# Performance work log

Measured on AMD Instinct MI355X. Metric: run time of the kernel, lower is better.

Reference implementation:

```python
import jax, jax.numpy as jnp
import numpy as np

B, S, D_IN, D_OUT = 4, 2048, 1024, 1024


def setup_inputs() -> dict:
    key = jax.random.key(0)
    ks = jax.random.split(key, 7)
    s_in = 1.0 / np.sqrt(D_IN)
    return {
        "x": jax.random.normal(ks[0], (B, S, D_IN), dtype=jnp.float32),
        "Wq": jax.random.uniform(ks[1], (D_IN, D_OUT), jnp.float32, -s_in, s_in),
        "bq": jax.random.uniform(ks[2], (D_OUT,), jnp.float32, -s_in, s_in),
        "Wk": jax.random.uniform(ks[3], (D_IN, D_OUT), jnp.float32, -s_in, s_in),
        "bk": jax.random.uniform(ks[4], (D_OUT,), jnp.float32, -s_in, s_in),
        "Wv": jax.random.uniform(ks[5], (D_IN, D_OUT), jnp.float32, -s_in, s_in),
        "bv": jax.random.uniform(ks[6], (D_OUT,), jnp.float32, -s_in, s_in),
    }


def reference(x, Wq, bq, Wk, bk, Wv, bv):
    # Linear projections (torch Linear: x @ W^T + b; here W stored as [in,out])
    q = x @ Wq + bq  # [B,S,D]
    k = x @ Wk + bk
    v = x @ Wv + bv
    scores = jnp.einsum("bqd,bkd->bqk", q, k)  # [B,S,S]
    # causal mask: positions j > i masked with -inf (applied BEFORE scaling,
    # which is equivalent since -inf/sqrt(d) == -inf)
    seq = scores.shape[-1]
    causal = jnp.tril(jnp.ones((seq, seq), dtype=bool))
    masked = jnp.where(causal, scores, -jnp.inf)
    attn = jax.nn.softmax(masked / np.sqrt(k.shape[-1]), axis=-1)
    # dropout p=0.0 -> identity
    return attn @ v  # [B,S,D]
```

## Files before the change

### kernel.cpp

```cpp
#include <hip/hip_runtime.h>

typedef unsigned short u16;
typedef unsigned int u32;
typedef __attribute__((ext_vector_type(8))) short short8;
typedef __attribute__((ext_vector_type(4))) float f32x4;

__device__ __forceinline__ u16 f2bf(float f) {
    u32 u = __float_as_uint(f);
    u32 r = (u + 0x7fffu + ((u >> 16) & 1u)) >> 16;
    return (u16)r;
}
__device__ __forceinline__ float bf2f(u16 h) {
    return __uint_as_float(((u32)h) << 16);
}

__device__ __forceinline__ void gld16(u16* lds_dst, const u16* g_src) {
    __builtin_amdgcn_global_load_lds(
        (const __attribute__((address_space(1))) unsigned int*)g_src,
        (__attribute__((address_space(3))) unsigned int*)lds_dst,
        16, 0, 0);
}

__global__ void split_x_k(const float* __restrict__ x, u16* __restrict__ xh,
                          u16* __restrict__ xl) {
    long i = ((long)blockIdx.x * 256 + threadIdx.x) * 4;
    float4 f = *(const float4*)(x + i);
    u16 h0 = f2bf(f.x), h1 = f2bf(f.y), h2 = f2bf(f.z), h3 = f2bf(f.w);
    u16 l0 = f2bf(f.x - bf2f(h0)), l1 = f2bf(f.y - bf2f(h1));
    u16 l2 = f2bf(f.z - bf2f(h2)), l3 = f2bf(f.w - bf2f(h3));
    uint2 hv, lv;
    hv.x = (u32)h0 | ((u32)h1 << 16); hv.y = (u32)h2 | ((u32)h3 << 16);
    lv.x = (u32)l0 | ((u32)l1 << 16); lv.y = (u32)l2 | ((u32)l3 << 16);
    *(uint2*)(xh + i) = hv;
    *(uint2*)(xl + i) = lv;
}

__global__ void splitT_w_k(const float* __restrict__ Wq, const float* __restrict__ Wk,
                           const float* __restrict__ Wv, u16* __restrict__ wth,
                           u16* __restrict__ wtl) {
    __shared__ float tile[32][33];
    int z = blockIdx.z;
    const float* W = (z == 0) ? Wq : (z == 1) ? Wk : Wv;
    int n0 = blockIdx.x * 32, k0 = blockIdx.y * 32;
    int tx = threadIdx.x, ty = threadIdx.y;
#pragma unroll
    for (int r0 = 0; r0 < 4; ++r0) {
        int r = ty + r0 * 8;
        tile[r][tx] = W[(long)(k0 + r) * 1024 + n0 + tx];
    }
    __syncthreads();
    long zoff = (long)z * 1024 * 1024;
#pragma unroll
    for (int r0 = 0; r0 < 4; ++r0) {
        int r = ty + r0 * 8;
        float f = tile[tx][r];
        u16 h = f2bf(f), l = f2bf(f - bf2f(h));
        long idx = zoff + (long)(n0 + r) * 1024 + k0 + tx;
        wth[idx] = h;
        wtl[idx] = l;
    }
}

__global__ void transpose_v_k(const u16* __restrict__ vh, const u16* __restrict__ vl,
                              u16* __restrict__ vth, u16* __restrict__ vtl) {
    __shared__ u16 th[32][33];
    __shared__ u16 tl[32][33];
    int z = blockIdx.z;
    int d0 = blockIdx.x * 32, s0 = blockIdx.y * 32;
    int tx = threadIdx.x, ty = threadIdx.y;
#pragma unroll
    for (int r0 = 0; r0 < 4; ++r0) {
        int r = ty + r0 * 8;
        long idx = ((long)z * 2048 + s0 + r) * 1024 + d0 + tx;
        th[r][tx] = vh[idx];
        tl[r][tx] = vl[idx];
    }
    __syncthreads();
    long zoff = (long)z * 1024 * 2048;
#pragma unroll
    for (int r0 = 0; r0 < 4; ++r0) {
        int r = ty + r0 * 8;
        long idx = zoff + (long)(d0 + r) * 2048 + s0 + tx;
        vth[idx] = th[tx][r];
        vtl[idx] = tl[tx][r];
    }
}

template <int MODE, int NF>
__launch_bounds__(512, 2)
__global__ void gemm_k(const u16* __restrict__ Ah, const u16* __restrict__ Al, long sAz,
                       const u16* __restrict__ Bh, const u16* __restrict__ Bl, long sBz,
                       int lda, int ldb, int Ksize,
                       float* __restrict__ outF, long sCz, int ldc,
                       u16* __restrict__ oh0, u16* __restrict__ oh1, u16* __restrict__ oh2,
                       u16* __restrict__ ol0, u16* __restrict__ ol1, u16* __restrict__ ol2,
                       const float* __restrict__ b0, const float* __restrict__ b1,
                       const float* __restrict__ b2) {
    constexpr int BN = NF * 64;
    constexpr int SLOT = 8192 + NF * 4096;
    __shared__ u16 lds[3 * SLOT];

    const int bi = blockIdx.x, bj = blockIdx.y, z = blockIdx.z;
    if (MODE == 1 && bj > bi) return;
    int nsteps = Ksize / 32;
    if (MODE == 2) nsteps = min(nsteps, (bi + 1) * 4);

    const u16* gA_h = Ah + (long)z * sAz;
    const u16* gA_l = Al + (long)z * sAz;
    const u16* gB_h = Bh + (long)z * sBz;
    const u16* gB_l = Bl + (long)z * sBz;

    const int tid = threadIdx.x;
    const int lane = tid & 63, w = tid >> 6;
    const int wr = w >> 2, wc = w & 3;

    const int srow = tid >> 2;
    const int ls8 = (((tid & 3) ^ ((tid >> 3) & 3)) << 3);
    const long aoff  = ((long)bi * 128 + srow) * lda + ls8;
    const long boff0 = ((long)bj * BN + srow) * ldb + ls8;
    const long boff1 = boff0 + 128L * (long)ldb;
    const int wbase = w * 512;

    f32x4 acc[4][NF] = {};

    const int fr = lane & 15;
    const int ps8 = (((lane >> 4) ^ ((fr >> 1) & 3)) << 3);

    auto stage = [&](int slot, int step) {
        const int k0 = step * 32;
        u16* sb = lds + slot * SLOT;
        gld16(sb + wbase,              gA_h + aoff + k0);
        gld16(sb + 4096 + wbase,       gA_l + aoff + k0);
        gld16(sb + 8192 + wbase,       gB_h + boff0 + k0);
        if constexpr (NF == 4) gld16(sb + 12288 + wbase, gB_h + boff1 + k0);
        gld16(sb + 8192 + NF * 2048 + wbase, gB_l + boff0 + k0);
        if constexpr (NF == 4) gld16(sb + 8192 + NF * 2048 + 4096 + wbase, gB_l + boff1 + k0);
    };

    auto compute = [&](int slot) {
        const u16* LA = lds + slot * SLOT;
        const u16* LB = LA + 8192;
        short8 afh[4], afl[4], bfh[NF], bfl[NF];
#pragma unroll
        for (int m = 0; m < 4; ++m) {
            int off = (wr * 64 + m * 16 + fr) * 32 + ps8;
            afh[m] = *(const short8*)(LA + off);
            afl[m] = *(const short8*)(LA + 4096 + off);
        }
#pragma unroll
        for (int n = 0; n < NF; ++n) {
            int off = (wc * (NF * 16) + n * 16 + fr) * 32 + ps8;
            bfh[n] = *(const short8*)(LB + off);
            bfl[n] = *(const short8*)(LB + NF * 2048 + off);
        }
        __builtin_amdgcn_s_setprio(1);
#pragma unroll
        for (int m = 0; m < 4; ++m)
#pragma unroll
            for (int n = 0; n < NF; ++n) {
                acc[m][n] = __builtin_amdgcn_mfma_f32_16x16x32_bf16(afh[m], bfh[n], acc[m][n], 0, 0, 0);
                acc[m][n] = __builtin_amdgcn_mfma_f32_16x16x32_bf16(afh[m], bfl[n], acc[m][n], 0, 0, 0);
                acc[m][n] = __builtin_amdgcn_mfma_f32_16x16x32_bf16(afl[m], bfh[n], acc[m][n], 0, 0, 0);
            }
        __builtin_amdgcn_s_setprio(0);
    };

    stage(0, 0);
    if (nsteps > 1) stage(1, 1);

    int cs = 0, ns = 2;
    for (int h = 0; h < nsteps; ++h) {
        if (h + 1 < nsteps) {
            if constexpr (NF == 4) asm volatile("s_waitcnt vmcnt(6)" ::: "memory");
            else                   asm volatile("s_waitcnt vmcnt(4)" ::: "memory");
        } else {
            asm volatile("s_waitcnt vmcnt(0)" ::: "memory");
        }
        __builtin_amdgcn_s_barrier();
        __builtin_amdgcn_sched_barrier(0);
        if (h + 2 < nsteps) stage(ns, h + 2);
        compute(cs);
        cs = (cs == 2) ? 0 : cs + 1;
        ns = (ns == 2) ? 0 : ns + 1;
    }

    const int row0 = bi * 128 + wr * 64 + (lane >> 4) * 4;
    const int col0 = bj * BN + wc * (NF * 16) + (lane & 15);

    if (MODE == 0) {
        const float* bias = (z == 0) ? b0 : (z == 1) ? b1 : b2;
        u16* oh = (z == 0) ? oh0 : (z == 1) ? oh1 : oh2;
        u16* ol = (z == 0) ? ol0 : (z == 1) ? ol1 : ol2;
#pragma unroll
        for (int n = 0; n < NF; ++n) {
            float bv = bias[col0 + n * 16];
#pragma unroll
            for (int m = 0; m < 4; ++m)
#pragma unroll
                for (int j = 0; j < 4; ++j) {
                    float v = acc[m][n][j] + bv;
                    long idx = (long)(row0 + m * 16 + j) * ldc + col0 + n * 16;
                    u16 h = f2bf(v);
                    oh[idx] = h;
                    ol[idx] = f2bf(v - bf2f(h));
                }
        }
    } else {
        float* o = outF + (long)z * sCz;
#pragma unroll
        for (int m = 0; m < 4; ++m)
#pragma unroll
            for (int n = 0; n < NF; ++n)
#pragma unroll
                for (int j = 0; j < 4; ++j)
                    o[(long)(row0 + m * 16 + j) * ldc + col0 + n * 16] = acc[m][n][j];
    }
}

__global__ void softmax_k(const float* __restrict__ S, u16* __restrict__ Ph,
                          u16* __restrict__ Pl) {
    const long row = blockIdx.x;
    const int i = (int)(row & 2047);
    const float* srow = S + row * 2048;
    u16* ph = Ph + row * 2048;
    u16* pl = Pl + row * 2048;
    const int t = threadIdx.x;
    const int limit = ((i >> 7) + 1) << 7;

    float v[8];
    float m = -1e30f;
#pragma unroll
    for (int j = 0; j < 8; ++j) {
        int c = j * 256 + t;
        float x = (c <= i) ? srow[c] : -1e30f;
        v[j] = x;
        m = fmaxf(m, x);
    }
#pragma unroll
    for (int off = 32; off; off >>= 1) m = fmaxf(m, __shfl_xor(m, off));
    __shared__ float redm[4], reds[4];
    if ((t & 63) == 0) redm[t >> 6] = m;
    __syncthreads();
    m = fmaxf(fmaxf(redm[0], redm[1]), fmaxf(redm[2], redm[3]));

    float p[8];
    float s = 0.f;
#pragma unroll
    for (int j = 0; j < 8; ++j) {
        int c = j * 256 + t;
        float e = (c <= i) ? __expf((v[j] - m) * 0.03125f) : 0.f;
        p[j] = e;
        s += e;
    }
#pragma unroll
    for (int off = 32; off; off >>= 1) s += __shfl_xor(s, off);
    if ((t & 63) == 0) reds[t >> 6] = s;
    __syncthreads();
    s = reds[0] + reds[1] + reds[2] + reds[3];
    const float inv = 1.f / s;
#pragma unroll
    for (int j = 0; j < 8; ++j) {
        int c = j * 256 + t;
        if (c < limit) {
            float o = p[j] * inv;
            u16 h = f2bf(o);
            ph[c] = h;
            pl[c] = f2bf(o - bf2f(h));
        }
    }
}

extern "C" void kernel_launch(void* const* d_in, const int* in_sizes, int n_in,
                              void* d_out, int out_size, void* d_ws, size_t ws_size,
                              hipStream_t stream) {
    const float* x  = (const float*)d_in[0];
    const float* Wq = (const float*)d_in[1];
    const float* bq = (const float*)d_in[2];
    const float* Wk = (const float*)d_in[3];
    const float* bk = (const float*)d_in[4];
    const float* Wv = (const float*)d_in[5];
    const float* bv = (const float*)d_in[6];
    float* out = (float*)d_out;
    char* ws = (char*)d_ws;
    const size_t MB = 1ull << 20;

    u16* xs_hi = (u16*)(ws + 0 * MB);
    u16* xs_lo = (u16*)(ws + 16 * MB);
    u16* wt_hi = (u16*)(ws + 32 * MB);
    u16* wt_lo = (u16*)(ws + 38 * MB);
    float* S   = (float*)(ws + 0 * MB);
    u16* q_hi = (u16*)(ws + 64 * MB);
    u16* q_lo = (u16*)(ws + 80 * MB);
    u16* k_hi = (u16*)(ws + 96 * MB);
    u16* k_lo = (u16*)(ws + 112 * MB);
    u16* P_hi = (u16*)(ws + 64 * MB);
    u16* P_lo = (u16*)(ws + 96 * MB);
    u16* v_hi  = (u16*)(ws + 128 * MB);
    u16* v_lo  = (u16*)(ws + 144 * MB);
    u16* vt_hi = (u16*)(ws + 160 * MB);
    u16* vt_lo = (u16*)(ws + 176 * MB);

    split_x_k<<<8192, 256, 0, stream>>>(x, xs_hi, xs_lo);
    splitT_w_k<<<dim3(32, 32, 3), dim3(32, 8), 0, stream>>>(Wq, Wk, Wv, wt_hi, wt_lo);
    gemm_k<0, 4><<<dim3(64, 4, 3), 512, 0, stream>>>(
        xs_hi, xs_lo, 0L, wt_hi, wt_lo, 1024L * 1024, 1024, 1024, 1024,
        nullptr, 0L, 1024, q_hi, k_hi, v_hi, q_lo, k_lo, v_lo, bq, bk, bv);
    transpose_v_k<<<dim3(32, 64, 4), dim3(32, 8), 0, stream>>>(v_hi, v_lo, vt_hi, vt_lo);
    gemm_k<1, 2><<<dim3(16, 16, 4), 512, 0, stream>>>(
        q_hi, q_lo, 2048L * 1024, k_hi, k_lo, 2048L * 1024, 1024, 1024, 1024,
        S, 2048L * 2048, 2048, nullptr, nullptr, nullptr, nullptr, nullptr, nullptr,
        nullptr, nullptr, nullptr);
    softmax_k<<<8192, 256, 0, stream>>>(S, P_hi, P_lo);
    gemm_k<2, 2><<<dim3(16, 8, 4), 512, 0, stream>>>(
        P_hi, P_lo, 2048L * 2048, vt_hi, vt_lo, 1024L * 2048, 2048, 2048, 2048,
        out, 2048L * 1024, 1024, nullptr, nullptr, nullptr, nullptr, nullptr, nullptr,
        nullptr, nullptr, nullptr);
}
```

Baseline: 468.4 us.

## Switch GEMM inner loop to 32x32x16 MFMA tiles and reverse PV block order

Replaces the 16x16x32 bf16 MFMA fragments with 32x32x16 instructions, which changes the per-wave register tiling, the LDS fragment read offsets, and the epilogue row/column mapping. Fewer, larger MFMAs mean fewer LDS fragment loads per FLOP. The causal PV GEMM now launches row blocks in reverse order so the longest (most K-steps) blocks start first, improving load balance. The risks are higher accumulator register pressure under the 512x2 launch bounds and different LDS bank patterns for the wider fragment reads.

Measured after the change: 505.9 us. +8.0%, slower.

```diff
diff --git a/kernel.cpp b/kernel.cpp
--- a/kernel.cpp
+++ b/kernel.cpp
@@ -3,7 +3,7 @@
 typedef unsigned short u16;
 typedef unsigned int u32;
 typedef __attribute__((ext_vector_type(8))) short short8;
-typedef __attribute__((ext_vector_type(4))) float f32x4;
+typedef __attribute__((ext_vector_type(16))) float f32x16;
 
 __device__ __forceinline__ u16 f2bf(float f) {
     u32 u = __float_as_uint(f);
@@ -86,7 +86,7 @@
     }
 }
 
-template <int MODE, int NF>
+template <int MODE, int BN>
 __launch_bounds__(512, 2)
 __global__ void gemm_k(const u16* __restrict__ Ah, const u16* __restrict__ Al, long sAz,
                        const u16* __restrict__ Bh, const u16* __restrict__ Bl, long sBz,
@@ -96,11 +96,15 @@
                        u16* __restrict__ ol0, u16* __restrict__ ol1, u16* __restrict__ ol2,
                        const float* __restrict__ b0, const float* __restrict__ b1,
                        const float* __restrict__ b2) {
-    constexpr int BN = NF * 64;
-    constexpr int SLOT = 8192 + NF * 4096;
+    constexpr int NFR = BN / 128;
+    constexpr int ASZ = 4096;
+    constexpr int BSZ = BN * 32;
+    constexpr int SLOT = 2 * ASZ + 2 * BSZ;
+    constexpr int NLOADS = (BN == 256) ? 6 : 4;
     __shared__ u16 lds[3 * SLOT];
 
-    const int bi = blockIdx.x, bj = blockIdx.y, z = blockIdx.z;
+    const int bi = (MODE == 2) ? (gridDim.x - 1 - (int)blockIdx.x) : blockIdx.x;
+    const int bj = blockIdx.y, z = blockIdx.z;
     if (MODE == 1 && bj > bi) return;
     int nsteps = Ksize / 32;
     if (MODE == 2) nsteps = min(nsteps, (bi + 1) * 4);
@@ -121,47 +125,62 @@
     const long boff1 = boff0 + 128L * (long)ldb;
     const int wbase = w * 512;
 
-    f32x4 acc[4][NF] = {};
-
-    const int fr = lane & 15;
-    const int ps8 = (((lane >> 4) ^ ((fr >> 1) & 3)) << 3);
+    f32x16 acc[2][NFR] = {};
+
+    const int r32 = lane & 31;
+    const int kg = (lane >> 5);
+
+    auto rdoff = [&](int row, int ks) {
+        int s = ks * 2 + kg;
+        return row * 32 + (((s ^ ((row >> 1) & 3))) << 3);
+    };
 
     auto stage = [&](int slot, int step) {
         const int k0 = step * 32;
         u16* sb = lds + slot * SLOT;
-        gld16(sb + wbase,              gA_h + aoff + k0);
-        gld16(sb + 4096 + wbase,       gA_l + aoff + k0);
-        gld16(sb + 8192 + wbase,       gB_h + boff0 + k0);
-        if constexpr (NF == 4) gld16(sb + 12288 + wbase, gB_h + boff1 + k0);
-        gld16(sb + 8192 + NF * 2048 + wbase, gB_l + boff0 + k0);
-        if constexpr (NF == 4) gld16(sb + 8192 + NF * 2048 + 4096 + wbase, gB_l + boff1 + k0);
+        gld16(sb + wbase,                 gA_h + aoff + k0);
+        gld16(sb + ASZ + wbase,           gA_l + aoff + k0);
+        gld16(sb + 2 * ASZ + wbase,       gB_h + boff0 + k0);
+        if constexpr (BN == 256) gld16(sb + 2 * ASZ + 4096 + wbase, gB_h + boff1 + k0);
+        gld16(sb + 2 * ASZ + BSZ + wbase, gB_l + boff0 + k0);
+        if constexpr (BN == 256) gld16(sb + 2 * ASZ + BSZ + 4096 + wbase, gB_l + boff1 + k0);
     };
 
     auto compute = [&](int slot) {
         const u16* LA = lds + slot * SLOT;
-        const u16* LB = LA + 8192;
-        short8 afh[4], afl[4], bfh[NF], bfl[NF];
-#pragma unroll
-        for (int m = 0; m < 4; ++m) {
-            int off = (wr * 64 + m * 16 + fr) * 32 + ps8;
-            afh[m] = *(const short8*)(LA + off);
-            afl[m] = *(const short8*)(LA + 4096 + off);
-        }
-#pragma unroll
-        for (int n = 0; n < NF; ++n) {
-            int off = (wc * (NF * 16) + n * 16 + fr) * 32 + ps8;
-            bfh[n] = *(const short8*)(LB + off);
-            bfl[n] = *(const short8*)(LB + NF * 2048 + off);
-        }
+        const u16* LB = LA + 2 * ASZ;
+        short8 a[2][2][2];
+        short8 b[NFR][2][2];
+#pragma unroll
+        for (int mf = 0; mf < 2; ++mf)
+#pragma unroll
+            for (int ks = 0; ks < 2; ++ks) {
+                int off = rdoff(wr * 64 + mf * 32 + r32, ks);
+                a[mf][ks][0] = *(const short8*)(LA + off);
+                a[mf][ks][1] = *(const short8*)(LA + ASZ + off);
+            }
+#pragma unroll
+        for (int nf = 0; nf < NFR; ++nf)
+#pragma unroll
+            for (int ks = 0; ks < 2; ++ks) {
+                int off = rdoff(wc * (NFR * 32) + nf * 32 + r32, ks);
+                b[nf][ks][0] = *(const short8*)(LB + off);
+                b[nf][ks][1] = *(const short8*)(LB + BSZ + off);
+            }
         __builtin_amdgcn_s_setprio(1);
 #pragma unroll
-        for (int m = 0; m < 4; ++m)
-#pragma unroll
-            for (int n = 0; n < NF; ++n) {
-                acc[m][n] = __builtin_amdgcn_mfma_f32_16x16x32_bf16(afh[m], bfh[n], acc[m][n], 0, 0, 0);
-                acc[m][n] = __builtin_amdgcn_mfma_f32_16x16x32_bf16(afh[m], bfl[n], acc[m][n], 0, 0, 0);
-                acc[m][n] = __builtin_amdgcn_mfma_f32_16x16x32_bf16(afl[m], bfh[n], acc[m][n], 0, 0, 0);
-            }
+        for (int ks = 0; ks < 2; ++ks)
+#pragma unroll
+            for (int mf = 0; mf < 2; ++mf)
+#pragma unroll
+                for (int nf = 0; nf < NFR; ++nf) {
+                    acc[mf][nf] = __builtin_amdgcn_mfma_f32_32x32x16_bf16(
+                        a[mf][ks][0], b[nf][ks][0], acc[mf][nf], 0, 0, 0);
+                    acc[mf][nf] = __builtin_amdgcn_mfma_f32_32x32x16_bf16(
+                        a[mf][ks][0], b[nf][ks][1], acc[mf][nf], 0, 0, 0);
+                    acc[mf][nf] = __builtin_amdgcn_mfma_f32_32x32x16_bf16(
+                        a[mf][ks][1], b[nf][ks][0], acc[mf][nf], 0, 0, 0);
+                }
         __builtin_amdgcn_s_setprio(0);
     };
 
@@ -171,8 +190,8 @@
     int cs = 0, ns = 2;
     for (int h = 0; h < nsteps; ++h) {
         if (h + 1 < nsteps) {
-            if constexpr (NF == 4) asm volatile("s_waitcnt vmcnt(6)" ::: "memory");
-            else                   asm volatile("s_waitcnt vmcnt(4)" ::: "memory");
+            if constexpr (BN == 256) asm volatile("s_waitcnt vmcnt(6)" ::: "memory");
+            else                     asm volatile("s_waitcnt vmcnt(4)" ::: "memory");
         } else {
             asm volatile("s_waitcnt vmcnt(0)" ::: "memory");
         }
@@ -184,22 +203,23 @@
         ns = (ns == 2) ? 0 : ns + 1;
     }
 
-    const int row0 = bi * 128 + wr * 64 + (lane >> 4) * 4;
-    const int col0 = bj * BN + wc * (NF * 16) + (lane & 15);
+    const int row0 = bi * 128 + wr * 64 + 4 * (lane >> 5);
+    const int col0 = bj * BN + wc * (NFR * 32) + r32;
 
     if (MODE == 0) {
         const float* bias = (z == 0) ? b0 : (z == 1) ? b1 : b2;
         u16* oh = (z == 0) ? oh0 : (z == 1) ? oh1 : oh2;
         u16* ol = (z == 0) ? ol0 : (z == 1) ? ol1 : ol2;
 #pragma unroll
-        for (int n = 0; n < NF; ++n) {
-            float bv = bias[col0 + n * 16];
-#pragma unroll
-            for (int m = 0; m < 4; ++m)
-#pragma unroll
-                for (int j = 0; j < 4; ++j) {
-                    float v = acc[m][n][j] + bv;
-                    long idx = (long)(row0 + m * 16 + j) * ldc + col0 + n * 16;
+        for (int nf = 0; nf < NFR; ++nf) {
+            float bv = bias[col0 + nf * 32];
+#pragma unroll
+            for (int mf = 0; mf < 2; ++mf)
+#pragma unroll
+                for (int j = 0; j < 16; ++j) {
+                    float v = acc[mf][nf][j] + bv;
+                    int row = row0 + mf * 32 + (j & 3) + 8 * (j >> 2);
+                    long idx = (long)row * ldc + col0 + nf * 32;
                     u16 h = f2bf(v);
                     oh[idx] = h;
                     ol[idx] = f2bf(v - bf2f(h));
@@ -208,12 +228,14 @@
     } else {
         float* o = outF + (long)z * sCz;
 #pragma unroll
-        for (int m = 0; m < 4; ++m)
-#pragma unroll
-            for (int n = 0; n < NF; ++n)
-#pragma unroll
-                for (int j = 0; j < 4; ++j)
-                    o[(long)(row0 + m * 16 + j) * ldc + col0 + n * 16] = acc[m][n][j];
+        for (int mf = 0; mf < 2; ++mf)
+#pragma unroll
+            for (int nf = 0; nf < NFR; ++nf)
+#pragma unroll
+                for (int j = 0; j < 16; ++j) {
+                    int row = row0 + mf * 32 + (j & 3) + 8 * (j >> 2);
+                    o[(long)row * ldc + col0 + nf * 32] = acc[mf][nf][j];
+                }
     }
 }
 
@@ -302,16 +324,16 @@
 
     split_x_k<<<8192, 256, 0, stream>>>(x, xs_hi, xs_lo);
     splitT_w_k<<<dim3(32, 32, 3), dim3(32, 8), 0, stream>>>(Wq, Wk, Wv, wt_hi, wt_lo);
-    gemm_k<0, 4><<<dim3(64, 4, 3), 512, 0, stream>>>(
+    gemm_k<0, 256><<<dim3(64, 4, 3), 512, 0, stream>>>(
         xs_hi, xs_lo, 0L, wt_hi, wt_lo, 1024L * 1024, 1024, 1024, 1024,
         nullptr, 0L, 1024, q_hi, k_hi, v_hi, q_lo, k_lo, v_lo, bq, bk, bv);
     transpose_v_k<<<dim3(32, 64, 4), dim3(32, 8), 0, stream>>>(v_hi, v_lo, vt_hi, vt_lo);
-    gemm_k<1, 2><<<dim3(16, 16, 4), 512, 0, stream>>>(
+    gemm_k<1, 128><<<dim3(16, 16, 4), 512, 0, stream>>>(
         q_hi, q_lo, 2048L * 1024, k_hi, k_lo, 2048L * 1024, 1024, 1024, 1024,
         S, 2048L * 2048, 2048, nullptr, nullptr, nullptr, nullptr, nullptr, nullptr,
         nullptr, nullptr, nullptr);
     softmax_k<<<8192, 256, 0, stream>>>(S, P_hi, P_lo);
-    gemm_k<2, 2><<<dim3(16, 8, 4), 512, 0, stream>>>(
+    gemm_k<2, 128><<<dim3(16, 8, 4), 512, 0, stream>>>(
         P_hi, P_lo, 2048L * 2048, vt_hi, vt_lo, 1024L * 2048, 2048, 2048, 2048,
         out, 2048L * 1024, 1024, nullptr, nullptr, nullptr, nullptr, nullptr, nullptr,
         nullptr, nullptr, nullptr);
```
